# Kernel optimization log

Hardware: AMD Instinct MI355X
Metric: run time of the kernel (lower is better)

Reference implementation:

```python
import jax, jax.numpy as jnp
import numpy as np

N_NODES = 50000
N_EDGES = 800000
F_IN = 64
F_OUT = 64
CUTOFF = 10.0


def _lin(key, fan_in, fan_out):
    kw, kb = jax.random.split(key)
    lim = 1.0 / np.sqrt(fan_in)
    W = jax.random.uniform(kw, (fan_in, fan_out), jnp.float32, -lim, lim)
    b = jax.random.uniform(kb, (fan_out,), jnp.float32, -lim, lim)
    return W, b


def setup_inputs() -> dict:
    key = jax.random.key(0)
    ks = jax.random.split(key, 8)
    x = jax.random.normal(ks[0], (N_NODES, F_IN), jnp.float32)
    edge_index = jax.random.randint(ks[1], (2, N_EDGES), 0, N_NODES, jnp.int32)
    pos = jax.random.uniform(ks[2], (N_NODES, 3), jnp.float32, 0.0, 20.0)
    Wp, bp = _lin(ks[3], F_IN, F_OUT)            # node_projection
    W1, b1 = _lin(ks[4], F_IN + 4, F_OUT)        # edge_mlp layer 1
    W2, b2 = _lin(ks[5], F_OUT, F_OUT)           # edge_mlp layer 2
    Wr1, br1 = _lin(ks[6], 1, 16)                # radial_func layer 1
    Wr2, br2 = _lin(ks[7], 16, 4)                # radial_func layer 2
    return {"x": x, "edge_index": edge_index, "pos": pos,
            "Wp": Wp, "bp": bp, "W1": W1, "b1": b1, "W2": W2, "b2": b2,
            "Wr1": Wr1, "br1": br1, "Wr2": Wr2, "br2": br2}


def reference(x, edge_index, pos, Wp, bp, W1, b1, W2, b2, Wr1, br1, Wr2, br2):
    src, tgt = edge_index[0], edge_index[1]
    rel_pos = pos[tgt] - pos[src]                               # [E, 3]
    d = jnp.linalg.norm(rel_pos, axis=-1, keepdims=True)        # [E, 1]
    edge_mask = (d < CUTOFF).astype(x.dtype)                    # [E, 1]
    # radial_func: Linear(1,16) -> SiLU -> Linear(16,4) -> SiLU
    radial = jax.nn.silu(jax.nn.silu(d @ Wr1 + br1) @ Wr2 + br2)  # [E, 4]
    # edge_mlp on [source_feats | radial]
    ef = jnp.concatenate([x[src], radial], axis=-1)             # [E, F_IN+4]
    ef = jax.nn.silu(jax.nn.silu(ef @ W1 + b1) @ W2 + b2)       # [E, F_OUT]
    # smooth cutoff; edges with d >= CUTOFF contribute exactly 0 (mask keeps
    # parity with the torch code's strict-< pre-filter)
    cutoff_factor = jnp.clip(1.0 - (d / CUTOFF) ** 2, 0.0, 1.0) * edge_mask
    ef = ef * cutoff_factor
    aggr = jax.ops.segment_sum(ef, tgt, num_segments=x.shape[0])  # [N, F_OUT]
    return x @ Wp + bp + aggr
```

## Files before the change

kernel.cpp:

```cpp
#include <hip/hip_runtime.h>
#include <hip/hip_bf16.h>
#include <math.h>

#define N_NODES 50000
#define N_EDGES 800000
#define F 64
#define CUTOFF2 100.0f

#define NPB 8
#define NBUCKET 6250
#define CAP 96
#define NODE_BLOCKS 782
#define PREP_BLOCKS 3125
#define MAIN_BLOCKS 1563

typedef __attribute__((ext_vector_type(8))) short    bf16x8;
typedef __attribute__((ext_vector_type(8))) _Float16 f16x8;
typedef __attribute__((ext_vector_type(4))) _Float16 f16x4;
typedef __attribute__((ext_vector_type(4))) float    f32x4;

__device__ __forceinline__ float silu_f(float v) {
    return v * __builtin_amdgcn_rcpf(1.0f + __expf(-v));
}

__device__ __forceinline__ unsigned short bf16_rne(float f) {
    unsigned int u = __float_as_uint(f);
    unsigned int r = (u + 0x7FFFu + ((u >> 16) & 1u)) >> 16;
    return (unsigned short)r;
}
__device__ __forceinline__ float bf16_f32(unsigned int h) {
    return __uint_as_float(h << 16);
}

__device__ __forceinline__ unsigned short f16_bits(float f) {
    _Float16 h = (_Float16)f;
    return __builtin_bit_cast(unsigned short, h);
}
__device__ __forceinline__ float f16_f32(unsigned short b) {
    return (float)__builtin_bit_cast(_Float16, b);
}

__device__ __forceinline__ f32x4 mfma16k_f16(f16x4 a, f16x4 b, f32x4 c) {
#if __has_builtin(__builtin_amdgcn_mfma_f32_16x16x16f16)
    return __builtin_amdgcn_mfma_f32_16x16x16f16(a, b, c, 0, 0, 0);
#elif __has_builtin(__builtin_amdgcn_mfma_f32_16x16x16_f16)
    return __builtin_amdgcn_mfma_f32_16x16x16_f16(a, b, c, 0, 0, 0);
#else
    f32x4 d = c;
    asm volatile("v_mfma_f32_16x16x16_f16 %0, %1, %2, %0"
                 : "+v"(d) : "v"(a), "v"(b));
    return d;
#endif
}

__device__ __forceinline__ void gemm16_store(
    const bf16x8 (&Ah)[2], const bf16x8 (&Al)[2],
    const float* __restrict__ W, const float* __restrict__ bias,
    float* __restrict__ dst, int n0, int r, int g)
{
    #pragma unroll
    for (int c = 0; c < 4; ++c) {
        f32x4 acc = {0.f, 0.f, 0.f, 0.f};
        #pragma unroll
        for (int t = 0; t < 2; ++t) {
            bf16x8 bh, bl;
            #pragma unroll
            for (int j = 0; j < 8; ++j) {
                const float wv = W[(size_t)(t * 32 + g * 8 + j) * F + c * 16 + r];
                const unsigned short hb = bf16_rne(wv);
                bh[j] = (short)hb;
                bl[j] = (short)bf16_rne(wv - bf16_f32(hb));
            }
            acc = __builtin_amdgcn_mfma_f32_16x16x32_bf16(Ah[t], bh, acc, 0, 0, 0);
            acc = __builtin_amdgcn_mfma_f32_16x16x32_bf16(Al[t], bh, acc, 0, 0, 0);
            acc = __builtin_amdgcn_mfma_f32_16x16x32_bf16(Ah[t], bl, acc, 0, 0, 0);
        }
        const float bb = bias[c * 16 + r];
        #pragma unroll
        for (int rg = 0; rg < 4; ++rg) {
            dst[(size_t)(n0 + g * 4 + rg) * F + c * 16 + r] = acc[rg] + bb;
        }
    }
}

__device__ __forceinline__ void gemm16_store_f16(
    const bf16x8 (&Ah)[2], const bf16x8 (&Al)[2],
    const float* __restrict__ W, const float* __restrict__ bias,
    _Float16* __restrict__ dst, int n0, int r, int g)
{
    #pragma unroll
    for (int c = 0; c < 4; ++c) {
        f32x4 acc = {0.f, 0.f, 0.f, 0.f};
        #pragma unroll
        for (int t = 0; t < 2; ++t) {
            bf16x8 bh, bl;
            #pragma unroll
            for (int j = 0; j < 8; ++j) {
                const float wv = W[(size_t)(t * 32 + g * 8 + j) * F + c * 16 + r];
                const unsigned short hb = bf16_rne(wv);
                bh[j] = (short)hb;
                bl[j] = (short)bf16_rne(wv - bf16_f32(hb));
            }
            acc = __builtin_amdgcn_mfma_f32_16x16x32_bf16(Ah[t], bh, acc, 0, 0, 0);
            acc = __builtin_amdgcn_mfma_f32_16x16x32_bf16(Al[t], bh, acc, 0, 0, 0);
            acc = __builtin_amdgcn_mfma_f32_16x16x32_bf16(Ah[t], bl, acc, 0, 0, 0);
        }
        const float bb = bias[c * 16 + r];
        #pragma unroll
        for (int rg = 0; rg < 4; ++rg) {
            dst[(size_t)(n0 + g * 4 + rg) * F + c * 16 + r] =
                (_Float16)(acc[rg] + bb);
        }
    }
}

__global__ __launch_bounds__(256) void node_prep_kernel(
    const float* __restrict__ x, const float* __restrict__ Wp,
    const float* __restrict__ bp, const float* __restrict__ W1,
    const float* __restrict__ b1,
    const int* __restrict__ ei, const float* __restrict__ pos,
    const float* __restrict__ Wr1, const float* __restrict__ br1,
    const float* __restrict__ Wr2, const float* __restrict__ br2,
    float* __restrict__ out, _Float16* __restrict__ h1,
    unsigned int* __restrict__ recs, int* __restrict__ counts)
{
    if (blockIdx.x < NODE_BLOCKS) {
        const int lane = threadIdx.x & 63;
        const int gw   = blockIdx.x * 4 + (threadIdx.x >> 6);
        if (gw >= N_NODES / 16) return;
        const int n0 = gw * 16;
        const int r = lane & 15, g = lane >> 4;

        bf16x8 Ah[2], Al[2];
        #pragma unroll
        for (int t = 0; t < 2; ++t) {
            const float* xp = x + (size_t)(n0 + r) * F + t * 32 + g * 8;
            #pragma unroll
            for (int j = 0; j < 8; ++j) {
                const float v = xp[j];
                const unsigned short hb = bf16_rne(v);
                Ah[t][j] = (short)hb;
                Al[t][j] = (short)bf16_rne(v - bf16_f32(hb));
            }
        }
        gemm16_store(Ah, Al, Wp, bp, out, n0, r, g);
        gemm16_store_f16(Ah, Al, W1, b1, h1, n0, r, g);
    } else {
        const int e = (blockIdx.x - NODE_BLOCKS) * 256 + threadIdx.x;
        const int src = ei[e];
        const int tgt = ei[N_EDGES + e];
        const float dx = pos[3 * tgt + 0] - pos[3 * src + 0];
        const float dy = pos[3 * tgt + 1] - pos[3 * src + 1];
        const float dz = pos[3 * tgt + 2] - pos[3 * src + 2];
        const float d2 = dx * dx + dy * dy + dz * dz;
        if (d2 >= CUTOFF2) return;

        const float d = sqrtf(d2);
        float a0 = br2[0], a1 = br2[1], a2 = br2[2], a3 = br2[3];
        #pragma unroll
        for (int i = 0; i < 16; ++i) {
            const float t = silu_f(fmaf(d, Wr1[i], br1[i]));
            a0 = fmaf(t, Wr2[i * 4 + 0], a0);
            a1 = fmaf(t, Wr2[i * 4 + 1], a1);
            a2 = fmaf(t, Wr2[i * 4 + 2], a2);
            a3 = fmaf(t, Wr2[i * 4 + 3], a3);
        }
        const float cut = 1.0f - d2 * 0.01f;

        const int b   = tgt >> 3;
        const int idx = atomicAdd(&counts[b], 1);
        if (idx < CAP) {
            uint4 rec;
            rec.x = (unsigned)src | ((unsigned)(tgt & 7) << 16);
            rec.y = (unsigned)f16_bits(silu_f(a0))
                  | ((unsigned)f16_bits(silu_f(a1)) << 16);
            rec.z = (unsigned)f16_bits(silu_f(a2))
                  | ((unsigned)f16_bits(silu_f(a3)) << 16);
            rec.w = __float_as_uint(cut);
            *(uint4*)(recs + ((size_t)b * CAP + idx) * 4) = rec;
        }
    }
}

struct TileIn {
    uint4 rec;
    f16x8 hA, hB;
};

__device__ __forceinline__ TileIn load_tile(
    const unsigned int* __restrict__ rbase, const _Float16* __restrict__ h1,
    int base, int r, int g, int cnt)
{
    TileIn ti;
    const int er = min(base + r, cnt - 1);
    ti.rec = *(const uint4*)(rbase + (size_t)er * 4);
    const int src = (int)(ti.rec.x & 0xFFFFu);
    const _Float16* hp = h1 + (size_t)src * F + g * 8;
    ti.hA = *(const f16x8*)(hp);
    ti.hB = *(const f16x8*)(hp + 32);
    return ti;
}

__global__ __launch_bounds__(256, 2) void edge_main_kernel(
    const unsigned int* __restrict__ recs, const int* __restrict__ counts,
    const _Float16* __restrict__ h1, const float* __restrict__ W1,
    const float* __restrict__ W2, const float* __restrict__ b2,
    float* __restrict__ out)
{
    const int lane = threadIdx.x & 63;
    const int w    = threadIdx.x >> 6;
    const int r    = lane & 15, g = lane >> 4;

    const int bkt = blockIdx.x * 4 + w;
    if (bkt >= NBUCKET) return;
    const int cnt = min(counts[bkt], CAP);
    if (cnt == 0) return;

    f16x8 Bh[4][2];
    #pragma unroll
    for (int c = 0; c < 4; ++c)
        #pragma unroll
        for (int t = 0; t < 2; ++t)
            #pragma unroll
            for (int jj = 0; jj < 8; ++jj)
                Bh[c][t][jj] = (_Float16)
                    W2[(size_t)(t * 32 + g * 8 + jj) * F + c * 16 + r];

    float w1r[4][2][8];
    #pragma unroll
    for (int i = 0; i < 4; ++i)
        #pragma unroll
        for (int t = 0; t < 2; ++t) {
            const float4 wa = *(const float4*)&W1[(size_t)(F + i) * F + t * 32 + g * 8];
            const float4 wb = *(const float4*)&W1[(size_t)(F + i) * F + t * 32 + g * 8 + 4];
            w1r[i][t][0] = wa.x; w1r[i][t][1] = wa.y;
            w1r[i][t][2] = wa.z; w1r[i][t][3] = wa.w;
            w1r[i][t][4] = wb.x; w1r[i][t][5] = wb.y;
            w1r[i][t][6] = wb.z; w1r[i][t][7] = wb.w;
        }

    float b2c[4];
    #pragma unroll
    for (int c = 0; c < 4; ++c) b2c[c] = b2[c * 16 + r];

    const int node0 = bkt * NPB;
    const unsigned int* rbase = recs + (size_t)bkt * CAP * 4;
    const int ntiles = (cnt + 15) >> 4;

    f32x4 acc3[4] = {};

    auto compute_tile = [&](const TileIn& ti, int base) {
        const int   lrow = (int)(ti.rec.x >> 16);
        const float rr0  = f16_f32((unsigned short)(ti.rec.y & 0xFFFFu));
        const float rr1  = f16_f32((unsigned short)(ti.rec.y >> 16));
        const float rr2  = f16_f32((unsigned short)(ti.rec.z & 0xFFFFu));
        const float rr3  = f16_f32((unsigned short)(ti.rec.z >> 16));
        const float cut  = __uint_as_float(ti.rec.w);

        int   lrow_e[4]; float cut_e[4];
        #pragma unroll
        for (int rg = 0; rg < 4; ++rg) {
            const int lr = __shfl(lrow, g * 4 + rg);
            lrow_e[rg] = (base + g * 4 + rg < cnt) ? lr : -1;
            cut_e[rg]  = __shfl(cut, g * 4 + rg);
        }

        f16x8 ah0, ah1;
        #pragma unroll
        for (int j = 0; j < 8; ++j) {
            float h0 = (float)ti.hA[j];
            h0 = fmaf(rr0, w1r[0][0][j], h0);
            h0 = fmaf(rr1, w1r[1][0][j], h0);
            h0 = fmaf(rr2, w1r[2][0][j], h0);
            h0 = fmaf(rr3, w1r[3][0][j], h0);
            ah0[j] = (_Float16)silu_f(h0);
            float h1v = (float)ti.hB[j];
            h1v = fmaf(rr0, w1r[0][1][j], h1v);
            h1v = fmaf(rr1, w1r[1][1][j], h1v);
            h1v = fmaf(rr2, w1r[2][1][j], h1v);
            h1v = fmaf(rr3, w1r[3][1][j], h1v);
            ah1[j] = (_Float16)silu_f(h1v);
        }

        f32x4 acc[4] = {};
        #pragma unroll
        for (int c = 0; c < 4; ++c) {
            acc[c] = __builtin_amdgcn_mfma_f32_16x16x32_f16(ah0, Bh[c][0], acc[c], 0, 0, 0);
            acc[c] = __builtin_amdgcn_mfma_f32_16x16x32_f16(ah1, Bh[c][1], acc[c], 0, 0, 0);
        }

        f16x4 afrag;
        afrag[0] = (lrow_e[0] == r) ? (_Float16)1.0f : (_Float16)0.0f;
        afrag[1] = (lrow_e[1] == r) ? (_Float16)1.0f : (_Float16)0.0f;
        afrag[2] = (lrow_e[2] == r) ? (_Float16)1.0f : (_Float16)0.0f;
        afrag[3] = (lrow_e[3] == r) ? (_Float16)1.0f : (_Float16)0.0f;

        #pragma unroll
        for (int c = 0; c < 4; ++c) {
            float ef[4];
            #pragma unroll
            for (int rg = 0; rg < 4; ++rg)
                ef[rg] = silu_f(acc[c][rg] + b2c[c]) * cut_e[rg];

            f16x4 beh, bel;
            #pragma unroll
            for (int rg = 0; rg < 4; ++rg) {
                const _Float16 hb = (_Float16)ef[rg];
                beh[rg] = hb;
                bel[rg] = (_Float16)(ef[rg] - (float)hb);
            }
            acc3[c] = mfma16k_f16(afrag, beh, acc3[c]);
            acc3[c] = mfma16k_f16(afrag, bel, acc3[c]);
        }
    };

    for (int s = 0; s < ntiles; s += 2) {
        const int baseA = s << 4;
        const int baseB = (s + 1) << 4;
        const TileIn tA = load_tile(rbase, h1, baseA, r, g, cnt);
        const TileIn tB = load_tile(rbase, h1, baseB, r, g, cnt);
        compute_tile(tA, baseA);
        compute_tile(tB, baseB);
    }

    if (g < 2) {
        #pragma unroll
        for (int rg = 0; rg < 4; ++rg) {
            float* rowp = out + (size_t)(node0 + g * 4 + rg) * F;
            #pragma unroll
            for (int c = 0; c < 4; ++c) {
                rowp[c * 16 + r] += acc3[c][rg];
            }
        }
    }
}

extern "C" void kernel_launch(void* const* d_in, const int* in_sizes, int n_in,
                              void* d_out, int out_size, void* d_ws, size_t ws_size,
                              hipStream_t stream) {
    const float* x   = (const float*)d_in[0];
    const int*   ei  = (const int*)d_in[1];
    const float* pos = (const float*)d_in[2];
    const float* Wp  = (const float*)d_in[3];
    const float* bp  = (const float*)d_in[4];
    const float* W1  = (const float*)d_in[5];
    const float* b1  = (const float*)d_in[6];
    const float* W2  = (const float*)d_in[7];
    const float* b2  = (const float*)d_in[8];
    const float* Wr1 = (const float*)d_in[9];
    const float* br1 = (const float*)d_in[10];
    const float* Wr2 = (const float*)d_in[11];
    const float* br2 = (const float*)d_in[12];
    float* out = (float*)d_out;

    char*         ws     = (char*)d_ws;
    int*          counts = (int*)ws;
    _Float16*     h1     = (_Float16*)(ws + 32768);
    unsigned int* recs   = (unsigned int*)(ws + 32768
                               + (size_t)N_NODES * F * sizeof(_Float16));

    hipMemsetAsync(counts, 0, NBUCKET * sizeof(int), stream);
    node_prep_kernel<<<NODE_BLOCKS + PREP_BLOCKS, 256, 0, stream>>>(
        x, Wp, bp, W1, b1, ei, pos, Wr1, br1, Wr2, br2,
        out, h1, recs, counts);
    edge_main_kernel<<<MAIN_BLOCKS, 256, 0, stream>>>(
        recs, counts, h1, W1, W2, b2, out);
}
```

Before: 65.05 us.

## Move node projection into edge kernel to seed accumulators, drop out read-modify-write

The x@Wp+bp projection moves out of the prep kernel and into the edge aggregation kernel. There it computes a 16-row tile per wave and uses the result as the initial value of the scatter accumulators. The final store then becomes a plain write instead of a read-modify-write of out, which removes one full write and one read of the output array. In exchange, each wave in the edge kernel does extra MFMA work on a 16-row tile while only 8 rows are used, which wastes half of it. The kernel also carries more register pressure before the edge loop.

Result: slower. 72.08 us (+10.8%).

```diff
diff --git a/kernel.cpp b/kernel.cpp
--- a/kernel.cpp
+++ b/kernel.cpp
@@ -53,75 +53,13 @@
 #endif
 }
 
-__device__ __forceinline__ void gemm16_store(
-    const bf16x8 (&Ah)[2], const bf16x8 (&Al)[2],
-    const float* __restrict__ W, const float* __restrict__ bias,
-    float* __restrict__ dst, int n0, int r, int g)
-{
-    #pragma unroll
-    for (int c = 0; c < 4; ++c) {
-        f32x4 acc = {0.f, 0.f, 0.f, 0.f};
-        #pragma unroll
-        for (int t = 0; t < 2; ++t) {
-            bf16x8 bh, bl;
-            #pragma unroll
-            for (int j = 0; j < 8; ++j) {
-                const float wv = W[(size_t)(t * 32 + g * 8 + j) * F + c * 16 + r];
-                const unsigned short hb = bf16_rne(wv);
-                bh[j] = (short)hb;
-                bl[j] = (short)bf16_rne(wv - bf16_f32(hb));
-            }
-            acc = __builtin_amdgcn_mfma_f32_16x16x32_bf16(Ah[t], bh, acc, 0, 0, 0);
-            acc = __builtin_amdgcn_mfma_f32_16x16x32_bf16(Al[t], bh, acc, 0, 0, 0);
-            acc = __builtin_amdgcn_mfma_f32_16x16x32_bf16(Ah[t], bl, acc, 0, 0, 0);
-        }
-        const float bb = bias[c * 16 + r];
-        #pragma unroll
-        for (int rg = 0; rg < 4; ++rg) {
-            dst[(size_t)(n0 + g * 4 + rg) * F + c * 16 + r] = acc[rg] + bb;
-        }
-    }
-}
-
-__device__ __forceinline__ void gemm16_store_f16(
-    const bf16x8 (&Ah)[2], const bf16x8 (&Al)[2],
-    const float* __restrict__ W, const float* __restrict__ bias,
-    _Float16* __restrict__ dst, int n0, int r, int g)
-{
-    #pragma unroll
-    for (int c = 0; c < 4; ++c) {
-        f32x4 acc = {0.f, 0.f, 0.f, 0.f};
-        #pragma unroll
-        for (int t = 0; t < 2; ++t) {
-            bf16x8 bh, bl;
-            #pragma unroll
-            for (int j = 0; j < 8; ++j) {
-                const float wv = W[(size_t)(t * 32 + g * 8 + j) * F + c * 16 + r];
-                const unsigned short hb = bf16_rne(wv);
-                bh[j] = (short)hb;
-                bl[j] = (short)bf16_rne(wv - bf16_f32(hb));
-            }
-            acc = __builtin_amdgcn_mfma_f32_16x16x32_bf16(Ah[t], bh, acc, 0, 0, 0);
-            acc = __builtin_amdgcn_mfma_f32_16x16x32_bf16(Al[t], bh, acc, 0, 0, 0);
-            acc = __builtin_amdgcn_mfma_f32_16x16x32_bf16(Ah[t], bl, acc, 0, 0, 0);
-        }
-        const float bb = bias[c * 16 + r];
-        #pragma unroll
-        for (int rg = 0; rg < 4; ++rg) {
-            dst[(size_t)(n0 + g * 4 + rg) * F + c * 16 + r] =
-                (_Float16)(acc[rg] + bb);
-        }
-    }
-}
-
 __global__ __launch_bounds__(256) void node_prep_kernel(
-    const float* __restrict__ x, const float* __restrict__ Wp,
-    const float* __restrict__ bp, const float* __restrict__ W1,
+    const float* __restrict__ x, const float* __restrict__ W1,
     const float* __restrict__ b1,
     const int* __restrict__ ei, const float* __restrict__ pos,
     const float* __restrict__ Wr1, const float* __restrict__ br1,
     const float* __restrict__ Wr2, const float* __restrict__ br2,
-    float* __restrict__ out, _Float16* __restrict__ h1,
+    _Float16* __restrict__ h1,
     unsigned int* __restrict__ recs, int* __restrict__ counts)
 {
     if (blockIdx.x < NODE_BLOCKS) {
@@ -143,8 +81,30 @@
                 Al[t][j] = (short)bf16_rne(v - bf16_f32(hb));
             }
         }
-        gemm16_store(Ah, Al, Wp, bp, out, n0, r, g);
-        gemm16_store_f16(Ah, Al, W1, b1, h1, n0, r, g);
+        #pragma unroll
+        for (int c = 0; c < 4; ++c) {
+            f32x4 acc = {0.f, 0.f, 0.f, 0.f};
+            #pragma unroll
+            for (int t = 0; t < 2; ++t) {
+                bf16x8 bh, bl;
+                #pragma unroll
+                for (int j = 0; j < 8; ++j) {
+                    const float wv = W1[(size_t)(t * 32 + g * 8 + j) * F + c * 16 + r];
+                    const unsigned short hb = bf16_rne(wv);
+                    bh[j] = (short)hb;
+                    bl[j] = (short)bf16_rne(wv - bf16_f32(hb));
+                }
+                acc = __builtin_amdgcn_mfma_f32_16x16x32_bf16(Ah[t], bh, acc, 0, 0, 0);
+                acc = __builtin_amdgcn_mfma_f32_16x16x32_bf16(Al[t], bh, acc, 0, 0, 0);
+                acc = __builtin_amdgcn_mfma_f32_16x16x32_bf16(Ah[t], bl, acc, 0, 0, 0);
+            }
+            const float bb = b1[c * 16 + r];
+            #pragma unroll
+            for (int rg = 0; rg < 4; ++rg) {
+                h1[(size_t)(n0 + g * 4 + rg) * F + c * 16 + r] =
+                    (_Float16)(acc[rg] + bb);
+            }
+        }
     } else {
         const int e = (blockIdx.x - NODE_BLOCKS) * 256 + threadIdx.x;
         const int src = ei[e];
@@ -205,6 +165,8 @@
     const unsigned int* __restrict__ recs, const int* __restrict__ counts,
     const _Float16* __restrict__ h1, const float* __restrict__ W1,
     const float* __restrict__ W2, const float* __restrict__ b2,
+    const float* __restrict__ x, const float* __restrict__ Wp,
+    const float* __restrict__ bp,
     float* __restrict__ out)
 {
     const int lane = threadIdx.x & 63;
@@ -214,113 +176,150 @@
     const int bkt = blockIdx.x * 4 + w;
     if (bkt >= NBUCKET) return;
     const int cnt = min(counts[bkt], CAP);
-    if (cnt == 0) return;
-
-    f16x8 Bh[4][2];
-    #pragma unroll
-    for (int c = 0; c < 4; ++c)
-        #pragma unroll
-        for (int t = 0; t < 2; ++t)
-            #pragma unroll
-            for (int jj = 0; jj < 8; ++jj)
-                Bh[c][t][jj] = (_Float16)
-                    W2[(size_t)(t * 32 + g * 8 + jj) * F + c * 16 + r];
-
-    float w1r[4][2][8];
-    #pragma unroll
-    for (int i = 0; i < 4; ++i)
+    const int node0 = bkt * NPB;
+
+    f32x4 acc3[4];
+    {
+        const int xrow = min(node0 + r, N_NODES - 1);
+        bf16x8 Ah[2], Al[2];
         #pragma unroll
         for (int t = 0; t < 2; ++t) {
-            const float4 wa = *(const float4*)&W1[(size_t)(F + i) * F + t * 32 + g * 8];
-            const float4 wb = *(const float4*)&W1[(size_t)(F + i) * F + t * 32 + g * 8 + 4];
-            w1r[i][t][0] = wa.x; w1r[i][t][1] = wa.y;
-            w1r[i][t][2] = wa.z; w1r[i][t][3] = wa.w;
-            w1r[i][t][4] = wb.x; w1r[i][t][5] = wb.y;
-            w1r[i][t][6] = wb.z; w1r[i][t][7] = wb.w;
-        }
-
-    float b2c[4];
-    #pragma unroll
-    for (int c = 0; c < 4; ++c) b2c[c] = b2[c * 16 + r];
-
-    const int node0 = bkt * NPB;
-    const unsigned int* rbase = recs + (size_t)bkt * CAP * 4;
-    const int ntiles = (cnt + 15) >> 4;
-
-    f32x4 acc3[4] = {};
-
-    auto compute_tile = [&](const TileIn& ti, int base) {
-        const int   lrow = (int)(ti.rec.x >> 16);
-        const float rr0  = f16_f32((unsigned short)(ti.rec.y & 0xFFFFu));
-        const float rr1  = f16_f32((unsigned short)(ti.rec.y >> 16));
-        const float rr2  = f16_f32((unsigned short)(ti.rec.z & 0xFFFFu));
-        const float rr3  = f16_f32((unsigned short)(ti.rec.z >> 16));
-        const float cut  = __uint_as_float(ti.rec.w);
-
-        int   lrow_e[4]; float cut_e[4];
-        #pragma unroll
-        for (int rg = 0; rg < 4; ++rg) {
-            const int lr = __shfl(lrow, g * 4 + rg);
-            lrow_e[rg] = (base + g * 4 + rg < cnt) ? lr : -1;
-            cut_e[rg]  = __shfl(cut, g * 4 + rg);
-        }
-
-        f16x8 ah0, ah1;
-        #pragma unroll
-        for (int j = 0; j < 8; ++j) {
-            float h0 = (float)ti.hA[j];
-            h0 = fmaf(rr0, w1r[0][0][j], h0);
-            h0 = fmaf(rr1, w1r[1][0][j], h0);
-            h0 = fmaf(rr2, w1r[2][0][j], h0);
-            h0 = fmaf(rr3, w1r[3][0][j], h0);
-            ah0[j] = (_Float16)silu_f(h0);
-            float h1v = (float)ti.hB[j];
-            h1v = fmaf(rr0, w1r[0][1][j], h1v);
-            h1v = fmaf(rr1, w1r[1][1][j], h1v);
-            h1v = fmaf(rr2, w1r[2][1][j], h1v);
-            h1v = fmaf(rr3, w1r[3][1][j], h1v);
-            ah1[j] = (_Float16)silu_f(h1v);
-        }
-
-        f32x4 acc[4] = {};
+            const float* xp = x + (size_t)xrow * F + t * 32 + g * 8;
+            #pragma unroll
+            for (int j = 0; j < 8; ++j) {
+                const float v = xp[j];
+                const unsigned short hb = bf16_rne(v);
+                Ah[t][j] = (short)hb;
+                Al[t][j] = (short)bf16_rne(v - bf16_f32(hb));
+            }
+        }
         #pragma unroll
         for (int c = 0; c < 4; ++c) {
-            acc[c] = __builtin_amdgcn_mfma_f32_16x16x32_f16(ah0, Bh[c][0], acc[c], 0, 0, 0);
-            acc[c] = __builtin_amdgcn_mfma_f32_16x16x32_f16(ah1, Bh[c][1], acc[c], 0, 0, 0);
-        }
-
-        f16x4 afrag;
-        afrag[0] = (lrow_e[0] == r) ? (_Float16)1.0f : (_Float16)0.0f;
-        afrag[1] = (lrow_e[1] == r) ? (_Float16)1.0f : (_Float16)0.0f;
-        afrag[2] = (lrow_e[2] == r) ? (_Float16)1.0f : (_Float16)0.0f;
-        afrag[3] = (lrow_e[3] == r) ? (_Float16)1.0f : (_Float16)0.0f;
-
-        #pragma unroll
-        for (int c = 0; c < 4; ++c) {
-            float ef[4];
-            #pragma unroll
-            for (int rg = 0; rg < 4; ++rg)
-                ef[rg] = silu_f(acc[c][rg] + b2c[c]) * cut_e[rg];
-
-            f16x4 beh, bel;
+            f32x4 a = {0.f, 0.f, 0.f, 0.f};
+            #pragma unroll
+            for (int t = 0; t < 2; ++t) {
+                bf16x8 bh, bl;
+                #pragma unroll
+                for (int j = 0; j < 8; ++j) {
+                    const float wv = Wp[(size_t)(t * 32 + g * 8 + j) * F + c * 16 + r];
+                    const unsigned short hb = bf16_rne(wv);
+                    bh[j] = (short)hb;
+                    bl[j] = (short)bf16_rne(wv - bf16_f32(hb));
+                }
+                a = __builtin_amdgcn_mfma_f32_16x16x32_bf16(Ah[t], bh, a, 0, 0, 0);
+                a = __builtin_amdgcn_mfma_f32_16x16x32_bf16(Al[t], bh, a, 0, 0, 0);
+                a = __builtin_amdgcn_mfma_f32_16x16x32_bf16(Ah[t], bl, a, 0, 0, 0);
+            }
+            const float bb = bp[c * 16 + r];
+            #pragma unroll
+            for (int rg = 0; rg < 4; ++rg) acc3[c][rg] = a[rg] + bb;
+        }
+    }
+
+    if (cnt > 0) {
+        f16x8 Bh[4][2];
+        #pragma unroll
+        for (int c = 0; c < 4; ++c)
+            #pragma unroll
+            for (int t = 0; t < 2; ++t)
+                #pragma unroll
+                for (int jj = 0; jj < 8; ++jj)
+                    Bh[c][t][jj] = (_Float16)
+                        W2[(size_t)(t * 32 + g * 8 + jj) * F + c * 16 + r];
+
+        float w1r[4][2][8];
+        #pragma unroll
+        for (int i = 0; i < 4; ++i)
+            #pragma unroll
+            for (int t = 0; t < 2; ++t) {
+                const float4 wa = *(const float4*)&W1[(size_t)(F + i) * F + t * 32 + g * 8];
+                const float4 wb = *(const float4*)&W1[(size_t)(F + i) * F + t * 32 + g * 8 + 4];
+                w1r[i][t][0] = wa.x; w1r[i][t][1] = wa.y;
+                w1r[i][t][2] = wa.z; w1r[i][t][3] = wa.w;
+                w1r[i][t][4] = wb.x; w1r[i][t][5] = wb.y;
+                w1r[i][t][6] = wb.z; w1r[i][t][7] = wb.w;
+            }
+
+        float b2c[4];
+        #pragma unroll
+        for (int c = 0; c < 4; ++c) b2c[c] = b2[c * 16 + r];
+
+        const unsigned int* rbase = recs + (size_t)bkt * CAP * 4;
+        const int ntiles = (cnt + 15) >> 4;
+
+        auto compute_tile = [&](const TileIn& ti, int base) {
+            const int   lrow = (int)(ti.rec.x >> 16);
+            const float rr0  = f16_f32((unsigned short)(ti.rec.y & 0xFFFFu));
+            const float rr1  = f16_f32((unsigned short)(ti.rec.y >> 16));
+            const float rr2  = f16_f32((unsigned short)(ti.rec.z & 0xFFFFu));
+            const float rr3  = f16_f32((unsigned short)(ti.rec.z >> 16));
+            const float cut  = __uint_as_float(ti.rec.w);
+
+            int   lrow_e[4]; float cut_e[4];
             #pragma unroll
             for (int rg = 0; rg < 4; ++rg) {
-                const _Float16 hb = (_Float16)ef[rg];
-                beh[rg] = hb;
-                bel[rg] = (_Float16)(ef[rg] - (float)hb);
-            }
-            acc3[c] = mfma16k_f16(afrag, beh, acc3[c]);
-            acc3[c] = mfma16k_f16(afrag, bel, acc3[c]);
-        }
-    };
-
-    for (int s = 0; s < ntiles; s += 2) {
-        const int baseA = s << 4;
-        const int baseB = (s + 1) << 4;
-        const TileIn tA = load_tile(rbase, h1, baseA, r, g, cnt);
-        const TileIn tB = load_tile(rbase, h1, baseB, r, g, cnt);
-        compute_tile(tA, baseA);
-        compute_tile(tB, baseB);
+                const int lr = __shfl(lrow, g * 4 + rg);
+                lrow_e[rg] = (base + g * 4 + rg < cnt) ? lr : -1;
+                cut_e[rg]  = __shfl(cut, g * 4 + rg);
+            }
+
+            f16x8 ah0, ah1;
+            #pragma unroll
+            for (int j = 0; j < 8; ++j) {
+                float h0 = (float)ti.hA[j];
+                h0 = fmaf(rr0, w1r[0][0][j], h0);
+                h0 = fmaf(rr1, w1r[1][0][j], h0);
+                h0 = fmaf(rr2, w1r[2][0][j], h0);
+                h0 = fmaf(rr3, w1r[3][0][j], h0);
+                ah0[j] = (_Float16)silu_f(h0);
+                float h1v = (float)ti.hB[j];
+                h1v = fmaf(rr0, w1r[0][1][j], h1v);
+                h1v = fmaf(rr1, w1r[1][1][j], h1v);
+                h1v = fmaf(rr2, w1r[2][1][j], h1v);
+                h1v = fmaf(rr3, w1r[3][1][j], h1v);
+                ah1[j] = (_Float16)silu_f(h1v);
+            }
+
+            f32x4 acc[4] = {};
+            #pragma unroll
+            for (int c = 0; c < 4; ++c) {
+                acc[c] = __builtin_amdgcn_mfma_f32_16x16x32_f16(ah0, Bh[c][0], acc[c], 0, 0, 0);
+                acc[c] = __builtin_amdgcn_mfma_f32_16x16x32_f16(ah1, Bh[c][1], acc[c], 0, 0, 0);
+            }
+
+            f16x4 afrag;
+            afrag[0] = (lrow_e[0] == r) ? (_Float16)1.0f : (_Float16)0.0f;
+            afrag[1] = (lrow_e[1] == r) ? (_Float16)1.0f : (_Float16)0.0f;
+            afrag[2] = (lrow_e[2] == r) ? (_Float16)1.0f : (_Float16)0.0f;
+            afrag[3] = (lrow_e[3] == r) ? (_Float16)1.0f : (_Float16)0.0f;
+
+            #pragma unroll
+            for (int c = 0; c < 4; ++c) {
+                float ef[4];
+                #pragma unroll
+                for (int rg = 0; rg < 4; ++rg)
+                    ef[rg] = silu_f(acc[c][rg] + b2c[c]) * cut_e[rg];
+
+                f16x4 beh, bel;
+                #pragma unroll
+                for (int rg = 0; rg < 4; ++rg) {
+                    const _Float16 hb = (_Float16)ef[rg];
+                    beh[rg] = hb;
+                    bel[rg] = (_Float16)(ef[rg] - (float)hb);
+                }
+                acc3[c] = mfma16k_f16(afrag, beh, acc3[c]);
+                acc3[c] = mfma16k_f16(afrag, bel, acc3[c]);
+            }
+        };
+
+        for (int s = 0; s < ntiles; s += 2) {
+            const int baseA = s << 4;
+            const int baseB = (s + 1) << 4;
+            const TileIn tA = load_tile(rbase, h1, baseA, r, g, cnt);
+            const TileIn tB = load_tile(rbase, h1, baseB, r, g, cnt);
+            compute_tile(tA, baseA);
+            compute_tile(tB, baseB);
+        }
     }
 
     if (g < 2) {
@@ -329,7 +328,7 @@
             float* rowp = out + (size_t)(node0 + g * 4 + rg) * F;
             #pragma unroll
             for (int c = 0; c < 4; ++c) {
-                rowp[c * 16 + r] += acc3[c][rg];
+                rowp[c * 16 + r] = acc3[c][rg];
             }
         }
     }
@@ -361,8 +360,7 @@
 
     hipMemsetAsync(counts, 0, NBUCKET * sizeof(int), stream);
     node_prep_kernel<<<NODE_BLOCKS + PREP_BLOCKS, 256, 0, stream>>>(
-        x, Wp, bp, W1, b1, ei, pos, Wr1, br1, Wr2, br2,
-        out, h1, recs, counts);
+        x, W1, b1, ei, pos, Wr1, br1, Wr2, br2, h1, recs, counts);
     edge_main_kernel<<<MAIN_BLOCKS, 256, 0, stream>>>(
-        recs, counts, h1, W1, W2, b2, out);
-}
+        recs, counts, h1, W1, W2, b2, x, Wp, bp, out);
+}
```
